# Kernel optimization log

Measured on AMD Instinct MI355X. Metric: run time of the kernel, lower is better.

The kernel has to match this reference:

```python
import jax, jax.numpy as jnp
import numpy as np
import math

N_HEADS = 16
EMBED_DIM = 1024
HEAD_DIM = EMBED_DIM // N_HEADS


def setup_inputs() -> dict:
    key = jax.random.key(0)
    k1, k2, k3 = jax.random.split(key, 3)
    bs, seq_len = 2, 2048
    x = jax.random.normal(k1, (bs, seq_len, EMBED_DIM), dtype=jnp.float32)
    # torch Linear weights are [out_features, in_features]
    W_in = jax.random.normal(k2, (3 * EMBED_DIM, EMBED_DIM), dtype=jnp.float32) * (1.0 / math.sqrt(EMBED_DIM))
    W_out = jax.random.normal(k3, (EMBED_DIM, EMBED_DIM), dtype=jnp.float32) * (1.0 / math.sqrt(EMBED_DIM))
    return {"x": x, "W_in": W_in, "W_out": W_out, "casual_mask": 1}


def reference(x, W_in, W_out, casual_mask):
    bs, seq_len, embed_dim = x.shape
    # fused QKV projection: x @ W_in.T -> [bs, seq, 3E]
    qkv = jnp.einsum('bse,fe->bsf', x, W_in)
    q, k, v = jnp.split(qkv, 3, axis=-1)
    # [bs, heads, seq, head_dim]
    def to_heads(t):
        return t.reshape(bs, seq_len, N_HEADS, HEAD_DIM).transpose(0, 2, 1, 3)
    q, k, v = to_heads(q), to_heads(k), to_heads(v)
    score = jnp.einsum('bhqd,bhkd->bhqk', q, k)
    if casual_mask:  # static Python flag
        causal = jnp.triu(jnp.ones((seq_len, seq_len), dtype=bool), k=1)
        score = jnp.where(causal, -jnp.inf, score)
    score = score / jnp.asarray(math.sqrt(HEAD_DIM), dtype=score.dtype)
    attn = jax.nn.softmax(score, axis=-1)
    out = jnp.einsum('bhqk,bhkd->bhqd', attn, v)
    out = out.transpose(0, 2, 1, 3).reshape(bs, seq_len, embed_dim)
    return jnp.einsum('bse,fe->bsf', out, W_out)
```

## Files before the change

kernel.cpp:

```cpp
#include <hip/hip_runtime.h>
#include <stdint.h>

#define SEQ 2048
#define BS 2
#define EMB 1024
#define NH 16
#define HD 64
#define F3 3072

using f32x4 = __attribute__((ext_vector_type(4))) float;
using bf16x8 = __attribute__((ext_vector_type(8))) short;

__device__ __forceinline__ unsigned short f2bf(float f) {
    union { float f; uint32_t u; } v; v.f = f;
    uint32_t u = v.u;
    u = u + 0x7FFFu + ((u >> 16) & 1u);
    return (unsigned short)(u >> 16);
}

__device__ __forceinline__ uint32_t pk_bf16(float a, float b) {
    uint32_t r;
    asm("v_cvt_pk_bf16_f32 %0, %1, %2" : "=v"(r) : "v"(a), "v"(b));
    return r;
}

#define GLOAD_LDS16(g, l) \
    __builtin_amdgcn_global_load_lds((const __attribute__((address_space(1))) void*)(g), \
                                     (__attribute__((address_space(3))) void*)(l), 16, 0, 0)

__global__ void cvt_kernel(const float* __restrict__ in, unsigned short* __restrict__ out, int n4) {
    int i = blockIdx.x * blockDim.x + threadIdx.x;
    if (i < n4) {
        f32x4 v = reinterpret_cast<const f32x4*>(in)[i];
        uint2 o;
        o.x = pk_bf16(v.x, v.y);
        o.y = pk_bf16(v.z, v.w);
        reinterpret_cast<uint2*>(out)[i] = o;
    }
}

template <bool BF16OUT>
__global__ __launch_bounds__(256) void gemm_bt(
    const unsigned short* __restrict__ A,
    const unsigned short* __restrict__ B,
    void* __restrict__ Cv,
    int M, int N, int K, int nbx)
{
    __shared__ unsigned short As[128 * 32];
    __shared__ unsigned short Bs[128 * 32];
    const int tid  = threadIdx.x;
    const int wave = tid >> 6, lane = tid & 63;
    const int wr = wave >> 1, wc = wave & 1;

    const int nwg = gridDim.x;
    const int s = (blockIdx.x & 7) * (nwg >> 3) + (blockIdx.x >> 3);
    const int bx = s % nbx, by = s / nbx;
    const int row0 = by * 128, col0 = bx * 128;

    f32x4 acc[4][4] = {};

    const int srow = wave * 16 + (lane >> 2);
    const int scol = (lane & 3) * 8;

    const unsigned short* gA = A + (size_t)(row0 + srow) * K + scol;
    const unsigned short* gB = B + (size_t)(col0 + srow) * K + scol;
    unsigned short* lA = As + wave * 16 * 32;
    unsigned short* lB = Bs + wave * 16 * 32;

    for (int kb = 0; kb < K; kb += 32) {
        __syncthreads();
        GLOAD_LDS16(gA + kb,                    lA);
        GLOAD_LDS16(gA + (size_t)64 * K + kb,   lA + 64 * 32);
        GLOAD_LDS16(gB + kb,                    lB);
        GLOAD_LDS16(gB + (size_t)64 * K + kb,   lB + 64 * 32);
        asm volatile("s_waitcnt vmcnt(0)" ::: "memory");
        __syncthreads();

        bf16x8 af[4], bfr[4];
#pragma unroll
        for (int mi = 0; mi < 4; mi++)
            af[mi] = *reinterpret_cast<const bf16x8*>(As + (wr * 64 + mi * 16 + (lane & 15)) * 32 + (lane >> 4) * 8);
#pragma unroll
        for (int ni = 0; ni < 4; ni++)
            bfr[ni] = *reinterpret_cast<const bf16x8*>(Bs + (wc * 64 + ni * 16 + (lane & 15)) * 32 + (lane >> 4) * 8);
#pragma unroll
        for (int mi = 0; mi < 4; mi++)
#pragma unroll
            for (int ni = 0; ni < 4; ni++)
                acc[mi][ni] = __builtin_amdgcn_mfma_f32_16x16x32_bf16(af[mi], bfr[ni], acc[mi][ni], 0, 0, 0);
    }

#pragma unroll
    for (int mi = 0; mi < 4; mi++)
#pragma unroll
        for (int ni = 0; ni < 4; ni++)
#pragma unroll
            for (int r = 0; r < 4; r++) {
                int row = row0 + wr * 64 + mi * 16 + (lane >> 4) * 4 + r;
                int col = col0 + wc * 64 + ni * 16 + (lane & 15);
                float v = acc[mi][ni][r];
                if constexpr (BF16OUT)
                    ((unsigned short*)Cv)[(size_t)row * N + col] = f2bf(v);
                else
                    ((float*)Cv)[(size_t)row * N + col] = v;
            }
}

__global__ __launch_bounds__(256) void attn_kernel(
    const unsigned short* __restrict__ qkv,
    unsigned short* __restrict__ ao)
{
    const int o = blockIdx.x;
    const int pos = o >> 3;
    const int bh = (o & 7) * 4 + (pos & 3);
    const int qb = 31 - (pos >> 2);
    const int b = bh >> 4, h = bh & 15;
    const int tid = threadIdx.x, wave = tid >> 6, lane = tid & 63;
    const int c = lane & 15, g = lane >> 4;

    __shared__ unsigned short Ks[64 * 64];
    __shared__ unsigned short Vs[64 * 64];
    __shared__ unsigned short Ps[4][16 * 64];

    const size_t base = (size_t)b * SEQ * F3;
    const int qrow0 = qb * 64 + wave * 16;
    const float SC = 0.18033688011f;

    bf16x8 qf[2];
#pragma unroll
    for (int sdq = 0; sdq < 2; sdq++) {
        int row = qrow0 + c;
        int d   = sdq * 32 + g * 8;
        qf[sdq] = *reinterpret_cast<const bf16x8*>(qkv + base + (size_t)row * F3 + h * HD + d);
    }

    f32x4 po[4] = {};
    float mR = -1e30f, lR = 0.f;

    const int ktiles = qb + 1;
    const int ksrow = tid >> 3;
    const int sch   = tid & 7;
    const int krow2 = (tid >> 3) * 2;

    const unsigned short* gK = qkv + base + EMB     + h * HD + sch * 8;
    const unsigned short* gV = qkv + base + 2 * EMB + h * HD + sch * 8;

    bf16x8 kp0 = *reinterpret_cast<const bf16x8*>(gK + (size_t)ksrow * F3);
    bf16x8 kp1 = *reinterpret_cast<const bf16x8*>(gK + (size_t)(32 + ksrow) * F3);
    bf16x8 vp0 = *reinterpret_cast<const bf16x8*>(gV + (size_t)krow2 * F3);
    bf16x8 vp1 = *reinterpret_cast<const bf16x8*>(gV + (size_t)(krow2 + 1) * F3);

    for (int kt_i = 0; kt_i < ktiles; kt_i++) {
        const int kbase = kt_i * 64;
        __syncthreads();
        {
            int off0 = (ksrow * 128 + sch * 16) ^ ((ksrow & 7) << 4);
            *reinterpret_cast<bf16x8*>((char*)Ks + off0) = kp0;
            int r1 = 32 + ksrow;
            int off1 = (r1 * 128 + sch * 16) ^ ((r1 & 7) << 4);
            *reinterpret_cast<bf16x8*>((char*)Ks + off1) = kp1;
        }
#pragma unroll
        for (int j = 0; j < 8; j++) {
            int d = sch * 8 + j;
            int off = (d * 128 + krow2 * 2) ^ ((((d & 7) ^ (d >> 3)) & 7) << 4);
            ushort2 pr; pr.x = (unsigned short)vp0[j]; pr.y = (unsigned short)vp1[j];
            *reinterpret_cast<ushort2*>((char*)Vs + off) = pr;
        }
        __syncthreads();

        if (kt_i + 1 < ktiles) {
            const int nb = kbase + 64;
            kp0 = *reinterpret_cast<const bf16x8*>(gK + (size_t)(nb + ksrow) * F3);
            kp1 = *reinterpret_cast<const bf16x8*>(gK + (size_t)(nb + 32 + ksrow) * F3);
            vp0 = *reinterpret_cast<const bf16x8*>(gV + (size_t)(nb + krow2) * F3);
            vp1 = *reinterpret_cast<const bf16x8*>(gV + (size_t)(nb + krow2 + 1) * F3);
        }

        f32x4 st[4] = {};
#pragma unroll
        for (int dstep = 0; dstep < 2; dstep++) {
            bf16x8 kf[4];
#pragma unroll
            for (int kt = 0; kt < 4; kt++) {
                int row = kt * 16 + c;
                int off = (row * 128 + dstep * 64 + g * 16) ^ ((row & 7) << 4);
                kf[kt] = *reinterpret_cast<const bf16x8*>((char*)Ks + off);
            }
#pragma unroll
            for (int kt = 0; kt < 4; kt++)
                st[kt] = __builtin_amdgcn_mfma_f32_16x16x32_bf16(kf[kt], qf[dstep], st[kt], 0, 0, 0);
        }

        const bool needmask = (kt_i == qb);
        {
            const int q = qrow0 + c;
            float mx = -3.0e38f;
#pragma unroll
            for (int kt = 0; kt < 4; kt++)
#pragma unroll
                for (int r = 0; r < 4; r++) {
                    float v = st[kt][r];
                    if (needmask) {
                        int k = kbase + kt * 16 + g * 4 + r;
                        if (k > q) v = -3.0e38f;
                    }
                    st[kt][r] = v;
                    mx = fmaxf(mx, v);
                }
            mx = fmaxf(mx, __shfl_xor(mx, 16));
            mx = fmaxf(mx, __shfl_xor(mx, 32));

            const bool skip = __all(mx - mR <= 8.0f);
            float mn = skip ? mR : fmaxf(mR, mx);
            const float nmn = -mn * SC;
            float rs = 0.f;
#pragma unroll
            for (int kt = 0; kt < 4; kt++)
#pragma unroll
                for (int r = 0; r < 4; r++) {
                    float p = __builtin_amdgcn_exp2f(__builtin_fmaf(st[kt][r], SC, nmn));
                    st[kt][r] = p;
                    rs += p;
                }
            rs += __shfl_xor(rs, 16);
            rs += __shfl_xor(rs, 32);
            if (skip) {
                lR += rs;
            } else {
                float alpha = __builtin_amdgcn_exp2f((mR - mn) * SC);
                mR = mn;
                lR = lR * alpha + rs;
#pragma unroll
                for (int r = 0; r < 4; r++) {
                    float ar = __shfl(alpha, (g << 2) + r);
#pragma unroll
                    for (int ni = 0; ni < 4; ni++) po[ni][r] *= ar;
                }
            }
        }

        unsigned short* Pw = Ps[wave];
        {
            int row = c;
#pragma unroll
            for (int kt = 0; kt < 4; kt++) {
                uint2 pk;
                pk.x = pk_bf16(st[kt][0], st[kt][1]);
                pk.y = pk_bf16(st[kt][2], st[kt][3]);
                int off = (row * 128 + kt * 32 + g * 8) ^ ((row & 7) << 4);
                *reinterpret_cast<uint2*>((char*)Pw + off) = pk;
            }
        }

#pragma unroll
        for (int s2 = 0; s2 < 2; s2++) {
            bf16x8 pa, vb[4];
            {
                int row = c;
                int off = (row * 128 + s2 * 64 + g * 16) ^ ((row & 7) << 4);
                pa = *reinterpret_cast<const bf16x8*>((char*)Pw + off);
            }
#pragma unroll
            for (int ni = 0; ni < 4; ni++) {
                int n = ni * 16 + c;
                int off = (n * 128 + s2 * 64 + g * 16) ^ ((((n & 7) ^ (n >> 3)) & 7) << 4);
                vb[ni] = *reinterpret_cast<const bf16x8*>((char*)Vs + off);
            }
#pragma unroll
            for (int ni = 0; ni < 4; ni++)
                po[ni] = __builtin_amdgcn_mfma_f32_16x16x32_bf16(pa, vb[ni], po[ni], 0, 0, 0);
        }
    }

    {
        float invl = 1.0f / lR;
#pragma unroll
        for (int r = 0; r < 4; r++) {
            float iv = __shfl(invl, (g << 2) + r);
            int row = qrow0 + g * 4 + r;
#pragma unroll
            for (int ni = 0; ni < 4; ni++) {
                int d = ni * 16 + c;
                ao[(size_t)(b * SEQ + row) * EMB + h * HD + d] = f2bf(po[ni][r] * iv);
            }
        }
    }
}

extern "C" void kernel_launch(void* const* d_in, const int* in_sizes, int n_in,
                              void* d_out, int out_size, void* d_ws, size_t ws_size,
                              hipStream_t stream)
{
    const float* x    = (const float*)d_in[0];
    const float* Win  = (const float*)d_in[1];
    const float* Wout = (const float*)d_in[2];
    float* out = (float*)d_out;

    char* ws = (char*)d_ws;
    unsigned short* xb    = (unsigned short*)(ws);
    unsigned short* winb  = (unsigned short*)(ws + (8u  << 20));
    unsigned short* woutb = (unsigned short*)(ws + (14u << 20));
    unsigned short* qkvb  = (unsigned short*)(ws + (16u << 20));
    unsigned short* aob   = (unsigned short*)(ws + (40u << 20));

    const int nx    = BS * SEQ * EMB;
    const int nwin  = F3 * EMB;
    const int nwout = EMB * EMB;

    cvt_kernel<<<nx    / 4 / 256, 256, 0, stream>>>(x,    xb,    nx / 4);
    cvt_kernel<<<nwin  / 4 / 256, 256, 0, stream>>>(Win,  winb,  nwin / 4);
    cvt_kernel<<<nwout / 4 / 256, 256, 0, stream>>>(Wout, woutb, nwout / 4);

    gemm_bt<true><<<dim3(768), 256, 0, stream>>>(xb, winb, (void*)qkvb, BS * SEQ, F3, EMB, F3 / 128);

    attn_kernel<<<dim3(1024), 256, 0, stream>>>(qkvb, aob);

    gemm_bt<false><<<dim3(256), 256, 0, stream>>>(aob, woutb, (void*)out, BS * SEQ, EMB, EMB, EMB / 128);
}
```

Before: 191.6 us.

## Double-buffer GEMM LDS tiles and write V transposed from QKV GEMM epilogue

The GEMM main loop now uses two LDS buffers, so the next K-slice's global-to-LDS loads are issued before the MFMAs on the current slice, overlapping memory latency with compute. The QKV GEMM epilogue writes the V block in a head-major transposed layout [b,h,d,s] into a separate buffer. The attention kernel can then stage V into LDS with vector stores instead of a scalar 8-way scatter transpose. The cost is doubled LDS per GEMM block, which may lower occupancy, plus a strided transposed-store epilogue in the GEMM.

```diff
diff --git a/kernel.cpp b/kernel.cpp
--- a/kernel.cpp
+++ b/kernel.cpp
@@ -39,22 +39,23 @@
     }
 }
 
-template <bool BF16OUT>
+template <bool QKV>
 __global__ __launch_bounds__(256) void gemm_bt(
     const unsigned short* __restrict__ A,
     const unsigned short* __restrict__ B,
     void* __restrict__ Cv,
+    unsigned short* __restrict__ vT,
     int M, int N, int K, int nbx)
 {
-    __shared__ unsigned short As[128 * 32];
-    __shared__ unsigned short Bs[128 * 32];
+    __shared__ unsigned short As[2][128 * 32];
+    __shared__ unsigned short Bs[2][128 * 32];
     const int tid  = threadIdx.x;
     const int wave = tid >> 6, lane = tid & 63;
     const int wr = wave >> 1, wc = wave & 1;
 
     const int nwg = gridDim.x;
-    const int s = (blockIdx.x & 7) * (nwg >> 3) + (blockIdx.x >> 3);
-    const int bx = s % nbx, by = s / nbx;
+    const int sw = (blockIdx.x & 7) * (nwg >> 3) + (blockIdx.x >> 3);
+    const int bx = sw % nbx, by = sw / nbx;
     const int row0 = by * 128, col0 = bx * 128;
 
     f32x4 acc[4][4] = {};
@@ -64,50 +65,85 @@
 
     const unsigned short* gA = A + (size_t)(row0 + srow) * K + scol;
     const unsigned short* gB = B + (size_t)(col0 + srow) * K + scol;
-    unsigned short* lA = As + wave * 16 * 32;
-    unsigned short* lB = Bs + wave * 16 * 32;
-
+    const int lofs = wave * 16 * 32;
+
+#define STAGE_G(buf, kb) do { \
+    GLOAD_LDS16(gA + (kb),                   As[buf] + lofs); \
+    GLOAD_LDS16(gA + (size_t)64 * K + (kb),  As[buf] + 64 * 32 + lofs); \
+    GLOAD_LDS16(gB + (kb),                   Bs[buf] + lofs); \
+    GLOAD_LDS16(gB + (size_t)64 * K + (kb),  Bs[buf] + 64 * 32 + lofs); } while (0)
+
+    STAGE_G(0, 0);
+    asm volatile("s_waitcnt vmcnt(0)" ::: "memory");
+    __syncthreads();
+
+    int cur = 0;
     for (int kb = 0; kb < K; kb += 32) {
-        __syncthreads();
-        GLOAD_LDS16(gA + kb,                    lA);
-        GLOAD_LDS16(gA + (size_t)64 * K + kb,   lA + 64 * 32);
-        GLOAD_LDS16(gB + kb,                    lB);
-        GLOAD_LDS16(gB + (size_t)64 * K + kb,   lB + 64 * 32);
+        if (kb + 32 < K) STAGE_G(cur ^ 1, kb + 32);
+
+        bf16x8 af[4], bfr[4];
+#pragma unroll
+        for (int mi = 0; mi < 4; mi++)
+            af[mi] = *reinterpret_cast<const bf16x8*>(As[cur] + (wr * 64 + mi * 16 + (lane & 15)) * 32 + (lane >> 4) * 8);
+#pragma unroll
+        for (int ni = 0; ni < 4; ni++)
+            bfr[ni] = *reinterpret_cast<const bf16x8*>(Bs[cur] + (wc * 64 + ni * 16 + (lane & 15)) * 32 + (lane >> 4) * 8);
+#pragma unroll
+        for (int mi = 0; mi < 4; mi++)
+#pragma unroll
+            for (int ni = 0; ni < 4; ni++)
+                acc[mi][ni] = __builtin_amdgcn_mfma_f32_16x16x32_bf16(af[mi], bfr[ni], acc[mi][ni], 0, 0, 0);
+
         asm volatile("s_waitcnt vmcnt(0)" ::: "memory");
         __syncthreads();
-
-        bf16x8 af[4], bfr[4];
+        cur ^= 1;
+    }
+#undef STAGE_G
+
+    if constexpr (QKV) {
+        if (col0 >= 2 * EMB) {
+#pragma unroll
+            for (int mi = 0; mi < 4; mi++)
+#pragma unroll
+                for (int ni = 0; ni < 4; ni++) {
+                    int vcol = col0 - 2 * EMB + wc * 64 + ni * 16 + (lane & 15);
+                    int hh = vcol >> 6, dd = vcol & 63;
+                    int row = row0 + wr * 64 + mi * 16 + (lane >> 4) * 4;
+                    int bb = row >> 11, ss = row & 2047;
+                    uint2 pk;
+                    pk.x = pk_bf16(acc[mi][ni][0], acc[mi][ni][1]);
+                    pk.y = pk_bf16(acc[mi][ni][2], acc[mi][ni][3]);
+                    *reinterpret_cast<uint2*>(vT + (size_t)((bb * 16 + hh) * 64 + dd) * 2048 + ss) = pk;
+                }
+        } else {
+#pragma unroll
+            for (int mi = 0; mi < 4; mi++)
+#pragma unroll
+                for (int ni = 0; ni < 4; ni++)
+#pragma unroll
+                    for (int r = 0; r < 4; r++) {
+                        int row = row0 + wr * 64 + mi * 16 + (lane >> 4) * 4 + r;
+                        int col = col0 + wc * 64 + ni * 16 + (lane & 15);
+                        ((unsigned short*)Cv)[(size_t)row * N + col] = f2bf(acc[mi][ni][r]);
+                    }
+        }
+    } else {
 #pragma unroll
         for (int mi = 0; mi < 4; mi++)
-            af[mi] = *reinterpret_cast<const bf16x8*>(As + (wr * 64 + mi * 16 + (lane & 15)) * 32 + (lane >> 4) * 8);
-#pragma unroll
-        for (int ni = 0; ni < 4; ni++)
-            bfr[ni] = *reinterpret_cast<const bf16x8*>(Bs + (wc * 64 + ni * 16 + (lane & 15)) * 32 + (lane >> 4) * 8);
-#pragma unroll
-        for (int mi = 0; mi < 4; mi++)
 #pragma unroll
             for (int ni = 0; ni < 4; ni++)
-                acc[mi][ni] = __builtin_amdgcn_mfma_f32_16x16x32_bf16(af[mi], bfr[ni], acc[mi][ni], 0, 0, 0);
-    }
-
-#pragma unroll
-    for (int mi = 0; mi < 4; mi++)
-#pragma unroll
-        for (int ni = 0; ni < 4; ni++)
-#pragma unroll
-            for (int r = 0; r < 4; r++) {
-                int row = row0 + wr * 64 + mi * 16 + (lane >> 4) * 4 + r;
-                int col = col0 + wc * 64 + ni * 16 + (lane & 15);
-                float v = acc[mi][ni][r];
-                if constexpr (BF16OUT)
-                    ((unsigned short*)Cv)[(size_t)row * N + col] = f2bf(v);
-                else
-                    ((float*)Cv)[(size_t)row * N + col] = v;
-            }
+#pragma unroll
+                for (int r = 0; r < 4; r++) {
+                    int row = row0 + wr * 64 + mi * 16 + (lane >> 4) * 4 + r;
+                    int col = col0 + wc * 64 + ni * 16 + (lane & 15);
+                    ((float*)Cv)[(size_t)row * N + col] = acc[mi][ni][r];
+                }
+    }
 }
 
 __global__ __launch_bounds__(256) void attn_kernel(
     const unsigned short* __restrict__ qkv,
+    const unsigned short* __restrict__ vT,
     unsigned short* __restrict__ ao)
 {
     const int o = blockIdx.x;
@@ -138,43 +174,39 @@
     float mR = -1e30f, lR = 0.f;
 
     const int ktiles = qb + 1;
-    const int ksrow = tid >> 3;
-    const int sch   = tid & 7;
-    const int krow2 = (tid >> 3) * 2;
-
-    const unsigned short* gK = qkv + base + EMB     + h * HD + sch * 8;
-    const unsigned short* gV = qkv + base + 2 * EMB + h * HD + sch * 8;
-
-    bf16x8 kp0 = *reinterpret_cast<const bf16x8*>(gK + (size_t)ksrow * F3);
-    bf16x8 kp1 = *reinterpret_cast<const bf16x8*>(gK + (size_t)(32 + ksrow) * F3);
-    bf16x8 vp0 = *reinterpret_cast<const bf16x8*>(gV + (size_t)krow2 * F3);
-    bf16x8 vp1 = *reinterpret_cast<const bf16x8*>(gV + (size_t)(krow2 + 1) * F3);
+    const int vrow = tid >> 3;
+    const int sch  = tid & 7;
+
+    const unsigned short* gK  = qkv + base + EMB + h * HD + sch * 8;
+    const unsigned short* gVT = vT + (size_t)bh * 64 * SEQ + sch * 8;
+
+    bf16x8 kp0 = *reinterpret_cast<const bf16x8*>(gK + (size_t)vrow * F3);
+    bf16x8 kp1 = *reinterpret_cast<const bf16x8*>(gK + (size_t)(32 + vrow) * F3);
+    bf16x8 vp0 = *reinterpret_cast<const bf16x8*>(gVT + (size_t)vrow * SEQ);
+    bf16x8 vp1 = *reinterpret_cast<const bf16x8*>(gVT + (size_t)(32 + vrow) * SEQ);
 
     for (int kt_i = 0; kt_i < ktiles; kt_i++) {
         const int kbase = kt_i * 64;
         __syncthreads();
         {
-            int off0 = (ksrow * 128 + sch * 16) ^ ((ksrow & 7) << 4);
+            int off0 = (vrow * 128 + sch * 16) ^ ((vrow & 7) << 4);
             *reinterpret_cast<bf16x8*>((char*)Ks + off0) = kp0;
-            int r1 = 32 + ksrow;
+            int r1 = 32 + vrow;
             int off1 = (r1 * 128 + sch * 16) ^ ((r1 & 7) << 4);
             *reinterpret_cast<bf16x8*>((char*)Ks + off1) = kp1;
-        }
-#pragma unroll
-        for (int j = 0; j < 8; j++) {
-            int d = sch * 8 + j;
-            int off = (d * 128 + krow2 * 2) ^ ((((d & 7) ^ (d >> 3)) & 7) << 4);
-            ushort2 pr; pr.x = (unsigned short)vp0[j]; pr.y = (unsigned short)vp1[j];
-            *reinterpret_cast<ushort2*>((char*)Vs + off) = pr;
+            int vo0 = (vrow * 128 + sch * 16) ^ ((((vrow & 7) ^ (vrow >> 3)) & 7) << 4);
+            *reinterpret_cast<bf16x8*>((char*)Vs + vo0) = vp0;
+            int vo1 = (r1 * 128 + sch * 16) ^ ((((r1 & 7) ^ (r1 >> 3)) & 7) << 4);
+            *reinterpret_cast<bf16x8*>((char*)Vs + vo1) = vp1;
         }
         __syncthreads();
 
         if (kt_i + 1 < ktiles) {
             const int nb = kbase + 64;
-            kp0 = *reinterpret_cast<const bf16x8*>(gK + (size_t)(nb + ksrow) * F3);
-            kp1 = *reinterpret_cast<const bf16x8*>(gK + (size_t)(nb + 32 + ksrow) * F3);
-            vp0 = *reinterpret_cast<const bf16x8*>(gV + (size_t)(nb + krow2) * F3);
-            vp1 = *reinterpret_cast<const bf16x8*>(gV + (size_t)(nb + krow2 + 1) * F3);
+            kp0 = *reinterpret_cast<const bf16x8*>(gK + (size_t)(nb + vrow) * F3);
+            kp1 = *reinterpret_cast<const bf16x8*>(gK + (size_t)(nb + 32 + vrow) * F3);
+            vp0 = *reinterpret_cast<const bf16x8*>(gVT + (size_t)vrow * SEQ + nb);
+            vp1 = *reinterpret_cast<const bf16x8*>(gVT + (size_t)(32 + vrow) * SEQ + nb);
         }
 
         f32x4 st[4] = {};
@@ -242,13 +274,12 @@
 
         unsigned short* Pw = Ps[wave];
         {
-            int row = c;
 #pragma unroll
             for (int kt = 0; kt < 4; kt++) {
                 uint2 pk;
                 pk.x = pk_bf16(st[kt][0], st[kt][1]);
                 pk.y = pk_bf16(st[kt][2], st[kt][3]);
-                int off = (row * 128 + kt * 32 + g * 8) ^ ((row & 7) << 4);
+                int off = (c * 128 + kt * 32 + g * 8) ^ ((c & 7) << 4);
                 *reinterpret_cast<uint2*>((char*)Pw + off) = pk;
             }
         }
@@ -257,8 +288,7 @@
         for (int s2 = 0; s2 < 2; s2++) {
             bf16x8 pa, vb[4];
             {
-                int row = c;
-                int off = (row * 128 + s2 * 64 + g * 16) ^ ((row & 7) << 4);
+                int off = (c * 128 + s2 * 64 + g * 16) ^ ((c & 7) << 4);
                 pa = *reinterpret_cast<const bf16x8*>((char*)Pw + off);
             }
 #pragma unroll
@@ -303,6 +333,7 @@
     unsigned short* woutb = (unsigned short*)(ws + (14u << 20));
     unsigned short* qkvb  = (unsigned short*)(ws + (16u << 20));
     unsigned short* aob   = (unsigned short*)(ws + (40u << 20));
+    unsigned short* vtb   = (unsigned short*)(ws + (48u << 20));
 
     const int nx    = BS * SEQ * EMB;
     const int nwin  = F3 * EMB;
@@ -312,9 +343,9 @@
     cvt_kernel<<<nwin  / 4 / 256, 256, 0, stream>>>(Win,  winb,  nwin / 4);
     cvt_kernel<<<nwout / 4 / 256, 256, 0, stream>>>(Wout, woutb, nwout / 4);
 
-    gemm_bt<true><<<dim3(768), 256, 0, stream>>>(xb, winb, (void*)qkvb, BS * SEQ, F3, EMB, F3 / 128);
-
-    attn_kernel<<<dim3(1024), 256, 0, stream>>>(qkvb, aob);
-
-    gemm_bt<false><<<dim3(256), 256, 0, stream>>>(aob, woutb, (void*)out, BS * SEQ, EMB, EMB, EMB / 128);
-}
+    gemm_bt<true><<<dim3(768), 256, 0, stream>>>(xb, winb, (void*)qkvb, vtb, BS * SEQ, F3, EMB, F3 / 128);
+
+    attn_kernel<<<dim3(1024), 256, 0, stream>>>(qkvb, vtb, aob);
+
+    gemm_bt<false><<<dim3(256), 256, 0, stream>>>(aob, woutb, (void*)out, nullptr, BS * SEQ, EMB, EMB, EMB / 128);
+}
```

Result: faster. 180.6 us (-5.7%).
